# Optimization experiments

Hardware: AMD Instinct MI355X
Metric: run time of the kernel (lower is better)

## Reference

```python
import jax, jax.numpy as jnp
import numpy as np

T = 1_048_576          # sequence length
NUM_INPUTS = 16        # symbol vocab for _delta table
MAX_OUTPUT = 25        # softmax width / counter range


def setup_inputs() -> dict:
    key = jax.random.key(0)
    k1, k2, k3 = jax.random.split(key, 3)
    input_seq = jax.random.randint(k1, (T,), 0, NUM_INPUTS)
    # learned params (random instead of the degenerate zero init so the
    # recurrence and softmax are non-trivial)
    delta = jax.random.normal(k2, (NUM_INPUTS,), dtype=jnp.float32) * 0.5
    out_bias = jax.random.normal(k3, (MAX_OUTPUT,), dtype=jnp.float32) * 0.1
    out_scale = jnp.ones((1,), dtype=jnp.float32)
    return {"input_seq": input_seq, "delta": delta,
            "out_bias": out_bias, "out_scale": out_scale}


def reference(input_seq, delta, out_bias, out_scale):
    max_out = out_bias.shape[0]
    # per-step increments: vectorized gather  [T]
    deltas = delta[input_seq]

    # scalar counter recurrence with clamp (non-associative -> lax.scan)
    def step(c, d):
        c = jnp.clip(c + d, 0.0, float(max_out - 1))
        return c, c

    _, counters = jax.lax.scan(step, jnp.float32(0.0), deltas)  # [T]

    # vectorized readout: distances [T, max_out] -> logits -> softmax
    positions = jnp.arange(max_out, dtype=jnp.float32)
    distances = jnp.abs(positions[None, :] - counters[:, None])
    logits = -distances * out_scale + out_bias
    return jax.nn.softmax(logits, axis=-1)  # [T, max_out]
```

## Files before the change

### kernel.cpp

```cpp
#include <hip/hip_runtime.h>

#define T_LEN   1048576
#define SEG     256
#define NSEG    (T_LEN / SEG)
#define MAXO    25
#define CLAMP_HI 24.0f
#define BIGF    1e30f

struct Trip { float a, l, h; };

__device__ __forceinline__ Trip comb(Trip x, Trip y) {
    Trip r;
    r.a = x.a + y.a;
    r.l = fmaxf(x.l + y.a, y.l);
    r.h = fminf(fmaxf(x.h + y.a, y.l), y.h);
    return r;
}
__device__ __forceinline__ float applyT(Trip p, float c) {
    return fminf(fmaxf(c + p.a, p.l), p.h);
}
__device__ __forceinline__ Trip shflUpTrip(Trip v, int off) {
    Trip r;
    r.a = __shfl_up(v.a, off, 64);
    r.l = __shfl_up(v.l, off, 64);
    r.h = __shfl_up(v.h, off, 64);
    return r;
}

__global__ __launch_bounds__(256)
void k1_seg(const int* __restrict__ seq, const float* __restrict__ delta,
            float* __restrict__ tri) {
    __shared__ float dl[16];
    const int tid = threadIdx.x, lane = tid & 63;
    if (tid < 16) dl[tid] = delta[tid];
    __syncthreads();

    const int4 s4 = *(const int4*)(seq + blockIdx.x * 1024 + tid * 4);
    Trip t = {dl[s4.x], 0.0f, CLAMP_HI};
    { Trip e = {dl[s4.y], 0.0f, CLAMP_HI}; t = comb(t, e); }
    { Trip e = {dl[s4.z], 0.0f, CLAMP_HI}; t = comb(t, e); }
    { Trip e = {dl[s4.w], 0.0f, CLAMP_HI}; t = comb(t, e); }

#pragma unroll
    for (int off = 1; off < 64; off <<= 1) {
        Trip o = shflUpTrip(t, off);
        if (lane >= off) t = comb(o, t);
    }
    if (lane == 63) {
        const int sid = blockIdx.x * 4 + (tid >> 6);
        tri[3 * sid + 0] = t.a;
        tri[3 * sid + 1] = t.l;
        tri[3 * sid + 2] = t.h;
    }
}

__global__ __launch_bounds__(1024)
void k2_scan(const float* __restrict__ tri, float* __restrict__ entry) {
    __shared__ Trip agg[16];
    const int tid = threadIdx.x, lane = tid & 63, wid = tid >> 6;

    const float4* p = (const float4*)(tri + tid * 12);
    const float4 f0 = p[0], f1 = p[1], f2 = p[2];
    const Trip t0 = {f0.x, f0.y, f0.z};
    const Trip t1 = {f0.w, f1.x, f1.y};
    const Trip t2 = {f1.z, f1.w, f2.x};
    const Trip t3 = {f2.y, f2.z, f2.w};

    Trip incl = comb(comb(comb(t0, t1), t2), t3);
#pragma unroll
    for (int off = 1; off < 64; off <<= 1) {
        Trip o = shflUpTrip(incl, off);
        if (lane >= off) incl = comb(o, incl);
    }
    if (lane == 63) agg[wid] = incl;
    __syncthreads();

    Trip W = {0.0f, -BIGF, BIGF};
    for (int w = 0; w < wid; ++w) W = comb(W, agg[w]);
    const Trip prev = shflUpTrip(incl, 1);
    const Trip E = (lane == 0) ? W : comb(W, prev);

    float c = applyT(E, 0.0f);
    entry[4 * tid + 0] = c;
    c = applyT(t0, c); entry[4 * tid + 1] = c;
    c = applyT(t1, c); entry[4 * tid + 2] = c;
    c = applyT(t2, c); entry[4 * tid + 3] = c;
}

__global__ __launch_bounds__(256)
void k3_out(const int* __restrict__ seq, const float* __restrict__ delta,
            const float* __restrict__ bias, const float* __restrict__ scale,
            const float* __restrict__ entry, float* __restrict__ out) {
    __shared__ float tile[SEG * MAXO];
    __shared__ Trip agg[4];
    __shared__ float dl[16], bs[MAXO];

    const int tid = threadIdx.x, lane = tid & 63, wid = tid >> 6;
    const int bid = blockIdx.x;

    if (tid < 16)   dl[tid] = delta[tid];
    if (tid < MAXO) bs[tid] = bias[tid];
    const float sfac = scale[0];
    const float cseg = entry[bid];
    const int s = seq[bid * SEG + tid];
    __syncthreads();

    Trip t = {dl[s], 0.0f, CLAMP_HI};
#pragma unroll
    for (int off = 1; off < 64; off <<= 1) {
        Trip o = shflUpTrip(t, off);
        if (lane >= off) t = comb(o, t);
    }
    if (lane == 63) agg[wid] = t;
    __syncthreads();

    float cb = cseg;
    for (int w = 0; w < wid; ++w) cb = applyT(agg[w], cb);
    const float c = applyT(t, cb);

    float ev[MAXO];
    float sum = 0.0f;
#pragma unroll
    for (int j = 0; j < MAXO; ++j) {
        ev[j] = __expf(fmaf(-sfac, fabsf((float)j - c), bs[j]));
        sum += ev[j];
    }
    const float r = 1.0f / sum;
#pragma unroll
    for (int j = 0; j < MAXO; ++j)
        tile[tid * MAXO + j] = ev[j] * r;
    __syncthreads();

    const float4* tp = (const float4*)tile;
    float4* op = (float4*)(out + (size_t)bid * SEG * MAXO);
#pragma unroll
    for (int i = tid; i < SEG * MAXO / 4; i += 256)
        op[i] = tp[i];
}

extern "C" void kernel_launch(void* const* d_in, const int* in_sizes, int n_in,
                              void* d_out, int out_size, void* d_ws, size_t ws_size,
                              hipStream_t stream) {
    const int*   seq   = (const int*)d_in[0];
    const float* delta = (const float*)d_in[1];
    const float* bias  = (const float*)d_in[2];
    const float* scale = (const float*)d_in[3];
    float* out = (float*)d_out;

    float* tri   = (float*)d_ws;
    float* entry = tri + NSEG * 3;

    k1_seg <<<T_LEN / 1024, 256, 0, stream>>>(seq, delta, tri);
    k2_scan<<<1, 1024, 0, stream>>>(tri, entry);
    k3_out <<<NSEG, 256, 0, stream>>>(seq, delta, bias, scale, entry, out);
}
```

Baseline: 123.8 us.

## Fuse segment reduction and global scan via last-block atomic; nontemporal output stores

Merges the per-segment triple reduction and the single-block global scan into one kernel. The last block to finish, detected with an atomic counter and threadfence, performs the scan, with each of 256 threads handling 16 segments. This removes one kernel launch and its dependency gap, but adds a memset launch and serialises the scan on one 256-thread block. The output copy in the readout kernel now uses nontemporal stores, to reduce cache pollution on the large streaming write.

Result: slower. 148.8 us (+20.2%).

```diff
diff --git a/kernel.cpp b/kernel.cpp
--- a/kernel.cpp
+++ b/kernel.cpp
@@ -1,11 +1,15 @@
 #include <hip/hip_runtime.h>
 
 #define T_LEN   1048576
+#define K1B     1024
+#define BLK     256
 #define SEG     256
 #define NSEG    (T_LEN / SEG)
 #define MAXO    25
 #define CLAMP_HI 24.0f
 #define BIGF    1e30f
+
+typedef float f4v __attribute__((ext_vector_type(4)));
 
 struct Trip { float a, l, h; };
 
@@ -27,15 +31,20 @@
     return r;
 }
 
-__global__ __launch_bounds__(256)
-void k1_seg(const int* __restrict__ seq, const float* __restrict__ delta,
-            float* __restrict__ tri) {
+__global__ __launch_bounds__(BLK)
+void k1_fused(const int* __restrict__ seq, const float* __restrict__ delta,
+              float* __restrict__ tri, float* __restrict__ entry,
+              int* __restrict__ cnt) {
     __shared__ float dl[16];
-    const int tid = threadIdx.x, lane = tid & 63;
+    __shared__ int isLast;
+    __shared__ Trip agg[4];
+    const int tid = threadIdx.x, lane = tid & 63, wid = tid >> 6;
+    const int bid = blockIdx.x;
+
     if (tid < 16) dl[tid] = delta[tid];
     __syncthreads();
 
-    const int4 s4 = *(const int4*)(seq + blockIdx.x * 1024 + tid * 4);
+    const int4 s4 = *(const int4*)(seq + bid * 1024 + tid * 4);
     Trip t = {dl[s4.x], 0.0f, CLAMP_HI};
     { Trip e = {dl[s4.y], 0.0f, CLAMP_HI}; t = comb(t, e); }
     { Trip e = {dl[s4.z], 0.0f, CLAMP_HI}; t = comb(t, e); }
@@ -47,26 +56,35 @@
         if (lane >= off) t = comb(o, t);
     }
     if (lane == 63) {
-        const int sid = blockIdx.x * 4 + (tid >> 6);
+        const int sid = bid * 4 + wid;
         tri[3 * sid + 0] = t.a;
         tri[3 * sid + 1] = t.l;
         tri[3 * sid + 2] = t.h;
     }
-}
+    __syncthreads();
+    if (tid == 0) {
+        __threadfence();
+        isLast = (atomicAdd(cnt, 1) == K1B - 1);
+    }
+    __syncthreads();
+    if (!isLast) return;
 
-__global__ __launch_bounds__(1024)
-void k2_scan(const float* __restrict__ tri, float* __restrict__ entry) {
-    __shared__ Trip agg[16];
-    const int tid = threadIdx.x, lane = tid & 63, wid = tid >> 6;
+    __threadfence();
+    f4v f[12];
+    const f4v* p = (const f4v*)(tri + tid * 48);
+#pragma unroll
+    for (int i = 0; i < 12; ++i) f[i] = p[i];
+    const float* fp = (const float*)f;
 
-    const float4* p = (const float4*)(tri + tid * 12);
-    const float4 f0 = p[0], f1 = p[1], f2 = p[2];
-    const Trip t0 = {f0.x, f0.y, f0.z};
-    const Trip t1 = {f0.w, f1.x, f1.y};
-    const Trip t2 = {f1.z, f1.w, f2.x};
-    const Trip t3 = {f2.y, f2.z, f2.w};
+    Trip loc[16];
+#pragma unroll
+    for (int k = 0; k < 16; ++k)
+        loc[k] = {fp[3 * k], fp[3 * k + 1], fp[3 * k + 2]};
 
-    Trip incl = comb(comb(comb(t0, t1), t2), t3);
+    Trip incl = loc[0];
+#pragma unroll
+    for (int k = 1; k < 16; ++k) incl = comb(incl, loc[k]);
+
 #pragma unroll
     for (int off = 1; off < 64; off <<= 1) {
         Trip o = shflUpTrip(incl, off);
@@ -80,18 +98,23 @@
     const Trip prev = shflUpTrip(incl, 1);
     const Trip E = (lane == 0) ? W : comb(W, prev);
 
+    float ebuf[16];
     float c = applyT(E, 0.0f);
-    entry[4 * tid + 0] = c;
-    c = applyT(t0, c); entry[4 * tid + 1] = c;
-    c = applyT(t1, c); entry[4 * tid + 2] = c;
-    c = applyT(t2, c); entry[4 * tid + 3] = c;
+    ebuf[0] = c;
+#pragma unroll
+    for (int k = 0; k < 15; ++k) { c = applyT(loc[k], c); ebuf[k + 1] = c; }
+
+    f4v* ep = (f4v*)(entry + 16 * tid);
+#pragma unroll
+    for (int i = 0; i < 4; ++i)
+        ep[i] = ((const f4v*)ebuf)[i];
 }
 
-__global__ __launch_bounds__(256)
-void k3_out(const int* __restrict__ seq, const float* __restrict__ delta,
+__global__ __launch_bounds__(BLK)
+void k2_out(const int* __restrict__ seq, const float* __restrict__ delta,
             const float* __restrict__ bias, const float* __restrict__ scale,
             const float* __restrict__ entry, float* __restrict__ out) {
-    __shared__ float tile[SEG * MAXO];
+    __shared__ __align__(16) float tile[SEG * MAXO];
     __shared__ Trip agg[4];
     __shared__ float dl[16], bs[MAXO];
 
@@ -131,11 +154,11 @@
         tile[tid * MAXO + j] = ev[j] * r;
     __syncthreads();
 
-    const float4* tp = (const float4*)tile;
-    float4* op = (float4*)(out + (size_t)bid * SEG * MAXO);
-#pragma unroll
-    for (int i = tid; i < SEG * MAXO / 4; i += 256)
-        op[i] = tp[i];
+    const f4v* tp = (const f4v*)tile;
+    f4v* op = (f4v*)(out + (size_t)bid * SEG * MAXO);
+#pragma unroll 4
+    for (int i = tid; i < SEG * MAXO / 4; i += BLK)
+        __builtin_nontemporal_store(tp[i], op + i);
 }
 
 extern "C" void kernel_launch(void* const* d_in, const int* in_sizes, int n_in,
@@ -149,8 +172,10 @@
 
     float* tri   = (float*)d_ws;
     float* entry = tri + NSEG * 3;
+    int*   cnt   = (int*)(entry + NSEG);
 
-    k1_seg <<<T_LEN / 1024, 256, 0, stream>>>(seq, delta, tri);
-    k2_scan<<<1, 1024, 0, stream>>>(tri, entry);
-    k3_out <<<NSEG, 256, 0, stream>>>(seq, delta, bias, scale, entry, out);
+    hipMemsetAsync(cnt, 0, sizeof(int), stream);
+
+    k1_fused<<<K1B, BLK, 0, stream>>>(seq, delta, tri, entry, cnt);
+    k2_out  <<<NSEG, BLK, 0, stream>>>(seq, delta, bias, scale, entry, out);
 }
```
